# Optimization experiments

Hardware: AMD Instinct MI355X
Metric: run time of the kernel (lower is better)

Reference implementation:

```python
import math
import jax, jax.numpy as jnp
import numpy as np

N, S, E, H = 8, 1024, 768, 12  # batch, seq_len, n_embed, n_head


def setup_inputs() -> dict:
    key = jax.random.key(0)
    ks = jax.random.split(key, 10)
    s = 1.0 / math.sqrt(E)
    x = jax.random.normal(ks[0], (N, S, E), dtype=jnp.float32)
    # per-head full-width projections, stacked over heads: [H, E, E] (Linear weight layout [out, in])
    Wq = jax.random.normal(ks[1], (H, E, E), dtype=jnp.float32) * s
    Wk = jax.random.normal(ks[2], (H, E, E), dtype=jnp.float32) * s
    Wv = jax.random.normal(ks[3], (H, E, E), dtype=jnp.float32) * s
    bq = jax.random.normal(ks[4], (H, E), dtype=jnp.float32) * s
    bk = jax.random.normal(ks[5], (H, E), dtype=jnp.float32) * s
    bv = jax.random.normal(ks[6], (H, E), dtype=jnp.float32) * s
    Wc = jax.random.normal(ks[7], (E, H * E), dtype=jnp.float32) * (1.0 / math.sqrt(H * E))
    bc = jax.random.normal(ks[8], (E,), dtype=jnp.float32) * s
    return {"x": x, "Wq": Wq, "bq": bq, "Wk": Wk, "bk": bk, "Wv": Wv, "bv": bv, "Wc": Wc, "bc": bc}


def reference(x, Wq, bq, Wk, bk, Wv, bv, Wc, bc):
    # Full-width QKV per head: [H, N, S, E]
    q = jnp.einsum('nse,hde->hnsd', x, Wq) + bq[:, None, None, :]
    k = jnp.einsum('nse,hde->hnsd', x, Wk) + bk[:, None, None, :]
    v = jnp.einsum('nse,hde->hnsd', x, Wv) + bv[:, None, None, :]
    # scores scaled by sqrt(n_embed) (source quirk: full n_embed, not head_dim)
    scores = jnp.einsum('hnsd,hntd->hnst', q, k) / math.sqrt(E)
    causal = jnp.tril(jnp.ones((S, S), dtype=bool))
    scores = jnp.where(causal[None, None, :, :], scores, -jnp.inf)
    # dropout applied before softmax in source; p=0 (eval) -> identity
    attn = jax.nn.softmax(scores, axis=-1)
    heads = jnp.einsum('hnst,hntd->hnsd', attn, v)  # [H, N, S, E]
    concat = jnp.transpose(heads, (1, 2, 0, 3)).reshape(N, S, H * E)
    return concat @ Wc.T + bc
```

## Files before the change

kernel.cpp:

```cpp
#include <hip/hip_runtime.h>
#include <hip/hip_bf16.h>
#include <stdint.h>

#define SEQ    1024
#define NBAT   8
#define EMB    768
#define NHEAD  12
#define MROWS  (NBAT*SEQ)
#define SCALE_S 0.03608439182435161f

typedef unsigned short u16;
typedef __attribute__((ext_vector_type(8))) short bf16x8;
typedef __attribute__((ext_vector_type(4))) float f32x4;

typedef void __attribute__((address_space(1)))* gas_ptr;
typedef void __attribute__((address_space(3)))* las_ptr;

__device__ __forceinline__ void gload16(const void* g, void* l) {
  __builtin_amdgcn_global_load_lds((gas_ptr)(void*)g, (las_ptr)l, 16, 0, 0);
}

#define VMCNT0 asm volatile("s_waitcnt vmcnt(0)" ::: "memory")
#define VMCNT2 asm volatile("s_waitcnt vmcnt(2)" ::: "memory")
#define VMCNT4 asm volatile("s_waitcnt vmcnt(4)" ::: "memory")
#define LGKM0  asm volatile("s_waitcnt lgkmcnt(0)" ::: "memory")
#define BARRIER asm volatile("s_barrier" ::: "memory")

__device__ __forceinline__ u16 f2bf(float f) {
  union { float f; uint32_t u; } a; a.f = f;
  uint32_t r = a.u + 0x7fffu + ((a.u >> 16) & 1u);
  return (u16)(r >> 16);
}
__device__ __forceinline__ float bf2f(u16 b) {
  union { uint32_t u; float f; } c; c.u = (uint32_t)b << 16; return c.f;
}
__device__ __forceinline__ uint32_t pack2(float a, float b) {
  return (uint32_t)f2bf(a) | ((uint32_t)f2bf(b) << 16);
}

__global__ void k_cvt(const float* __restrict__ s, u16* __restrict__ d, long n) {
  long i = ((long)blockIdx.x*blockDim.x + threadIdx.x)*8;
  if (i >= n) return;
  float4 a = *(const float4*)(s+i);
  float4 b = *(const float4*)(s+i+4);
  uint4 o; o.x = pack2(a.x,a.y); o.y = pack2(a.z,a.w);
  o.z = pack2(b.x,b.y); o.w = pack2(b.z,b.w);
  *(uint4*)(d+i) = o;
}

__global__ void k_cvtT(const float* __restrict__ wq, const float* __restrict__ wk,
                       u16* __restrict__ dq, u16* __restrict__ dk, int Gi) {
  __shared__ float t[64][65];
  int z = blockIdx.z;
  const float* src = (z < Gi) ? wq + (size_t)z*EMB*EMB : wk + (size_t)(z-Gi)*EMB*EMB;
  u16* dst = (z < Gi) ? dq + (size_t)z*EMB*EMB : dk + (size_t)(z-Gi)*EMB*EMB;
  int d0 = blockIdx.x*64, e0 = blockIdx.y*64;
  int tt = threadIdx.x;
  int el = tt & 63, db = tt >> 6;
  #pragma unroll
  for (int p = 0; p < 16; ++p) {
    int dl = p*4 + db;
    t[dl][el] = src[(size_t)(d0+dl)*EMB + e0 + el];
  }
  __syncthreads();
  int dl2 = tt & 63, eb = tt >> 6;
  #pragma unroll
  for (int p = 0; p < 16; ++p) {
    int e2 = p*4 + eb;
    dst[(size_t)(e0+e2)*EMB + d0 + dl2] = f2bf(t[dl2][e2]);
  }
}

__global__ void k_cvtwc(const float* __restrict__ wc, u16* __restrict__ d, int Gi, int h0) {
  long ncol = (long)Gi*EMB;
  long i = ((long)blockIdx.x*blockDim.x + threadIdx.x)*4;
  if (i >= 768*ncol) return;
  long eo = i / ncol, c = i - eo*ncol;
  long g = c / EMB, dd = c - g*EMB;
  const float* s = wc + eo*(long)(NHEAD*EMB) + (h0+g)*EMB + dd;
  float4 a = *(const float4*)s;
  uint2 o; o.x = pack2(a.x,a.y); o.y = pack2(a.z,a.w);
  *(uint2*)(d+i) = o;
}

__global__ void k_mka(const u16* __restrict__ wkT, const float* __restrict__ bq,
                      float* __restrict__ a) {
  int g = blockIdx.y;
  int e = blockIdx.x*256 + threadIdx.x;
  const u16* row = wkT + (size_t)g*EMB*EMB + (size_t)e*EMB;
  const float* b = bq + (size_t)g*EMB;
  float s = 0.f;
  for (int d = 0; d < EMB; ++d) s += bf2f(row[d]) * b[d];
  a[(size_t)g*EMB + e] = s;
}

__global__ void k_mkv(const u16* __restrict__ xb, const float* __restrict__ a,
                      float* __restrict__ v) {
  int g = blockIdx.y;
  int w = threadIdx.x >> 6, l = threadIdx.x & 63;
  int i = blockIdx.x*8 + w;
  const u16* xr = xb + (size_t)i*EMB;
  const float* ag = a + (size_t)g*EMB;
  float s = 0.f;
  #pragma unroll
  for (int c = 0; c < 12; ++c) {
    int e = c*64 + l;
    s += bf2f(xr[e]) * ag[e];
  }
  s += __shfl_xor(s, 1); s += __shfl_xor(s, 2); s += __shfl_xor(s, 4);
  s += __shfl_xor(s, 8); s += __shfl_xor(s, 16); s += __shfl_xor(s, 32);
  if (l == 0) v[(size_t)g*MROWS + i] = s;
}

__global__ __launch_bounds__(512, 2) void k_gemm256(
    const u16* __restrict__ A, int lda,
    const u16* __restrict__ B, int ldb, int K,
    u16* __restrict__ Cb, long c_hs, int ldc,
    const float* __restrict__ bias, const float* __restrict__ bias2,
    int gsplit, int mode)
{
  __shared__ u16 lsA[2*16384];
  __shared__ u16 lsB[2*16384];

  int m0 = blockIdx.x * 256;
  int n0 = blockIdx.y * 256;
  int tid = threadIdx.x;
  int w = tid >> 6, l = tid & 63;
  int wr = w >> 2, wc = w & 3;

  const u16* gA = A + (size_t)(m0 + 32*w + (l>>3))*lda + (((l&7) ^ (l>>3)) << 3);
  const u16* gB = B + (size_t)(n0 + 32*w + (l>>3))*ldb + (((l&7) ^ (l>>3)) << 3);

#define STAGE256(t, buf) do { \
    int k0_ = (t)*64; \
    _Pragma("unroll") \
    for (int c_ = 0; c_ < 4; ++c_) \
      gload16(gA + (size_t)(c_*8)*lda + k0_, lsA + (buf)*16384 + (32*w + 8*c_)*64); \
    _Pragma("unroll") \
    for (int c_ = 0; c_ < 4; ++c_) \
      gload16(gB + (size_t)(c_*8)*ldb + k0_, lsB + (buf)*16384 + (32*w + 8*c_)*64); \
  } while(0)

  f32x4 acc[8][4];
  #pragma unroll
  for (int i = 0; i < 8; ++i)
    #pragma unroll
    for (int j = 0; j < 4; ++j) acc[i][j] = (f32x4)0.0f;

  int nt = K >> 6;
  STAGE256(0, 0);
  for (int t = 0; t < nt; ++t) {
    VMCNT0; BARRIER;
    if (t + 1 < nt) STAGE256(t+1, (t+1)&1);
    const u16* la = lsA + (t&1)*16384;
    const u16* lb = lsB + (t&1)*16384;
    #pragma unroll
    for (int ks = 0; ks < 2; ++ks) {
      int off = (((4*ks + (l>>4)) ^ (l&7)) << 3);
      bf16x8 af[8], bf_[4];
      #pragma unroll
      for (int fi = 0; fi < 8; ++fi)
        af[fi] = *(const bf16x8*)(la + (wr*128 + fi*16 + (l&15))*64 + off);
      #pragma unroll
      for (int fj = 0; fj < 4; ++fj)
        bf_[fj] = *(const bf16x8*)(lb + (wc*64 + fj*16 + (l&15))*64 + off);
      __builtin_amdgcn_s_setprio(1);
      #pragma unroll
      for (int fi = 0; fi < 8; ++fi)
        #pragma unroll
        for (int fj = 0; fj < 4; ++fj)
          acc[fi][fj] = __builtin_amdgcn_mfma_f32_16x16x32_bf16(af[fi], bf_[fj], acc[fi][fj], 0, 0, 0);
      __builtin_amdgcn_s_setprio(0);
    }
  }
#undef STAGE256

  if (mode == 0) {
    int s = n0 / 768;
    int dbase = n0 - s*768 + wc*64;
    const float* bsl = bias ? ((s < gsplit) ? bias + (size_t)s*768
                                            : bias2 + (size_t)(s - gsplit)*768)
                            : (const float*)0;
    u16* Cs = Cb + (size_t)s*c_hs;
    #pragma unroll
    for (int fj = 0; fj < 4; ++fj) {
      int dcol = dbase + fj*16 + (l&15);
      float bb = bsl ? bsl[dcol] : 0.f;
      #pragma unroll
      for (int fi = 0; fi < 8; ++fi) {
        #pragma unroll
        for (int r = 0; r < 4; ++r) {
          int row = m0 + wr*128 + fi*16 + (l>>4)*4 + r;
          Cs[(size_t)row*768 + dcol] = f2bf(acc[fi][fj][r] + bb);
        }
      }
    }
  } else {
    #pragma unroll
    for (int fi = 0; fi < 8; ++fi) {
      #pragma unroll
      for (int r = 0; r < 4; ++r) {
        int row = m0 + wr*128 + fi*16 + (l>>4)*4 + r;
        float bb = bias[row];
        #pragma unroll
        for (int fj = 0; fj < 4; ++fj) {
          int cbn = n0 + wc*64 + fj*16 + (l&15);
          Cb[(size_t)row*ldc + cbn] = f2bf(acc[fi][fj][r] + bb);
        }
      }
    }
  }
}

__global__ __launch_bounds__(256) void k_gemm(
    const u16* __restrict__ A, long a_hs, int lda,
    const u16* __restrict__ B, long b_hs, int ldb, int K,
    u16* Cb, float* Cf, long c_hs, int ldc,
    const float* __restrict__ bias, const float* __restrict__ bias2,
    long bias_hs, int gsplit, int mode, int swapxy)
{
  __shared__ u16 lsA[3*4096];
  __shared__ u16 lsB[3*4096];
  int g = blockIdx.z;
  const u16* Ag = A + (long)g*a_hs;
  const u16* Bg = B + (long)g*b_hs;
  int tm = swapxy ? blockIdx.y : blockIdx.x;
  int tn = swapxy ? blockIdx.x : blockIdx.y;
  int m0 = tm*128, n0 = tn*128;
  int tid = threadIdx.x;
  int w = tid >> 6, l = tid & 63;

  int srow = l >> 2;
  int scol = ((l & 3) ^ ((l >> 3) & 3)) * 8;
  const u16* ga0 = Ag + (long)(m0 + (2*w)*16   + srow)*lda + scol;
  const u16* ga1 = Ag + (long)(m0 + (2*w+1)*16 + srow)*lda + scol;
  const u16* gb0 = Bg + (long)(n0 + (2*w)*16   + srow)*ldb + scol;
  const u16* gb1 = Bg + (long)(n0 + (2*w+1)*16 + srow)*ldb + scol;

#define GSTAGE(k0, buf) do { \
    gload16(ga0 + (k0), lsA + (buf)*4096 + (2*w)*512); \
    gload16(ga1 + (k0), lsA + (buf)*4096 + (2*w+1)*512); \
    gload16(gb0 + (k0), lsB + (buf)*4096 + (2*w)*512); \
    gload16(gb1 + (k0), lsB + (buf)*4096 + (2*w+1)*512); \
  } while(0)

  f32x4 acc[4][4];
  #pragma unroll
  for (int i = 0; i < 4; ++i)
    #pragma unroll
    for (int j = 0; j < 4; ++j) acc[i][j] = (f32x4)0.0f;

  int wr = w >> 1, wc_ = w & 1;
  int frow = l & 15;
  int sp = (l >> 4) ^ ((frow >> 1) & 3);
  int aoff[4], boff[4];
  #pragma unroll
  for (int i = 0; i < 4; ++i) {
    aoff[i] = (wr*64 + i*16 + frow)*32 + sp*8;
    boff[i] = (wc_*64 + i*16 + frow)*32 + sp*8;
  }

  int nt = K >> 5;
  GSTAGE(0, 0);
  GSTAGE(32, 1);
  VMCNT4; BARRIER;
  int cur = 0;
  for (int t = 0; t < nt; ++t) {
    if (t + 2 < nt) {
      int nb = cur + 2; if (nb >= 3) nb -= 3;
      GSTAGE((t+2) << 5, nb);
    }
    const u16* la = lsA + cur*4096;
    const u16* lb = lsB + cur*4096;
    bf16x8 af[4], bfr[4];
    #pragma unroll
    for (int i = 0; i < 4; ++i) af[i] = *(const bf16x8*)(la + aoff[i]);
    #pragma unroll
    for (int j = 0; j < 4; ++j) bfr[j] = *(const bf16x8*)(lb + boff[j]);
    #pragma unroll
    for (int i = 0; i < 4; ++i)
      #pragma unroll
      for (int j = 0; j < 4; ++j)
        acc[i][j] = __builtin_amdgcn_mfma_f32_16x16x32_bf16(af[i], bfr[j], acc[i][j], 0, 0, 0);
    if (t + 2 < nt) { VMCNT4; } else { VMCNT0; }
    LGKM0; BARRIER;
    cur = (cur == 2) ? 0 : cur + 1;
  }
#undef GSTAGE

  u16* Cbg = Cb ? Cb + (long)g*c_hs : (u16*)0;
  const float* bsel = (g < gsplit) ? bias : bias2;
  long gi = (g < gsplit) ? g : g - gsplit;
  const float* bs = bsel ? bsel + gi*bias_hs : (const float*)0;
  int rl = (l >> 4)*4, cl = l & 15;
  #pragma unroll
  for (int i = 0; i < 4; ++i) {
    #pragma unroll
    for (int j = 0; j < 4; ++j) {
      int rb = m0 + wr*64 + i*16 + rl;
      int cb = n0 + wc_*64 + j*16 + cl;
      float cbv = 0.f;
      if ((mode == 0 || mode == 2) && bs) cbv = bs[cb];
      #pragma unroll
      for (int r = 0; r < 4; ++r) {
        int rr = rb + r;
        float v = acc[i][j][r];
        v += (mode == 1) ? bs[rr] : cbv;
        size_t idx = (size_t)rr*(size_t)ldc + cb;
        if (mode <= 1) Cbg[idx] = f2bf(v);
        else if (mode == 2) Cf[idx] = v;
        else Cf[idx] += v;
      }
    }
  }
}

__global__ __launch_bounds__(512, 2) void k_attn(
    const u16* __restrict__ qb, const u16* __restrict__ xkb,
    const u16* __restrict__ vtb, const float* __restrict__ vh,
    u16* __restrict__ hb, int ldh)
{
  __shared__ u16 kls[3*8192];
  __shared__ u16 vls[3*8192];
  __shared__ float s_t[64*68];
  __shared__ u16 p_t[64*64];
  __shared__ float e_s[64];

  int b = blockIdx.x;
  int xcd = b & 7, kk_ = b >> 3;
  int gn = xcd + 8*(kk_ >> 3), pair = kk_ & 7;
  int g = gn >> 3, n = gn & 7;

  const u16* Q  = qb  + (size_t)g*MROWS*EMB + (size_t)n*SEQ*EMB;
  const u16* Kp = xkb + (size_t)n*SEQ*EMB;
  const u16* Vt = vtb + (size_t)g*EMB*MROWS + (size_t)n*SEQ;
  const float* Vh = vh + (size_t)g*MROWS + (size_t)n*SEQ;
  u16* H = hb + (size_t)(n*SEQ)*ldh + (size_t)g*EMB;

  int tid = threadIdx.x;
  int w = tid >> 6, l = tid & 63;
  int qg = w >> 1;
  int cg = w & 1;
  int frow = l & 15;
  int fsw = frow & 7;
  int srow = tid >> 3;
  int sphys = tid & 7;
  int scol = ((sphys ^ (srow & 7)) << 3);

#define KSTAGE(base, pc, buf) do { \
    gload16((base) + (pc)*128,      kls + (buf)*8192 + w*512); \
    gload16((base) + (pc)*128 + 64, kls + (buf)*8192 + 4096 + w*512); \
  } while(0)
#define VSTAGE(vc, buf) do { \
    gload16(Vs + (size_t)((vc)*128)*MROWS,      vls + (buf)*8192 + w*512); \
    gload16(Vs + (size_t)((vc)*128 + 64)*MROWS, vls + (buf)*8192 + 4096 + w*512); \
  } while(0)

  for (int half = 0; half < 2; ++half) {
    int qt = half ? 15 - pair : pair;
    int q0 = qt * 64;
    int nt = qt + 1;

    f32x4 acc[6][4];
    #pragma unroll
    for (int i = 0; i < 6; ++i)
      #pragma unroll
      for (int j = 0; j < 4; ++j) acc[i][j] = (f32x4)0.0f;
    float m_reg = -1e30f, l_reg = 0.f;

    const u16* Qs = Q + (size_t)(q0 + srow)*EMB + scol;
    bf16x8 qreg[12][2];
    KSTAGE(Qs, 0, 0);
    KSTAGE(Qs, 1, 1);
    VMCNT2; BARRIER;
    #pragma unroll
    for (int pc = 0; pc < 6; ++pc) {
      if (pc < 4) KSTAGE(Qs, pc+2, (pc+2)%3);
      const u16* qb_ = kls + (pc%3)*8192;
      #pragma unroll
      for (int kk2 = 0; kk2 < 2; ++kk2)
        #pragma unroll
        for (int kkl = 0; kkl < 2; ++kkl)
          qreg[2*pc + kk2][kkl] = *(const bf16x8*)(qb_ + kk2*4096 + (qg*16 + frow)*64
                                                   + (((kkl*4 + (l>>4)) ^ fsw) << 3));
      if (pc < 4) { VMCNT2; } else if (pc == 4) { VMCNT0; }
      LGKM0; BARRIER;
    }

    for (int tt = 0; tt < nt; ++tt) {
      int t0 = tt*64;
      const u16* Ks = Kp + (size_t)(t0 + srow)*EMB + scol;
      const u16* Vs = Vt + (size_t)srow*MROWS + t0 + scol;
      float vv0 = Vh[t0 + cg*32 + frow];
      float vv1 = Vh[t0 + cg*32 + 16 + frow];
      if (tt == 0) { KSTAGE(Ks, 0, 0); KSTAGE(Ks, 1, 1); }
      VMCNT2; BARRIER;

      f32x4 sacc[2]; sacc[0] = (f32x4)0.0f; sacc[1] = (f32x4)0.0f;
      #pragma unroll
      for (int c = 0; c < 6; ++c) {
        if (c < 4)       KSTAGE(Ks, c+2, (c+2)%3);
        else if (c == 4) VSTAGE(0, 0);
        else             VSTAGE(1, 1);
        const u16* kb_ = kls + (c%3)*8192;
        __builtin_amdgcn_s_setprio(1);
        #pragma unroll
        for (int kk2 = 0; kk2 < 2; ++kk2) {
          #pragma unroll
          for (int kkl = 0; kkl < 2; ++kkl) {
            int so = ((kkl*4 + (l>>4)) ^ fsw) << 3;
            bf16x8 aq = qreg[2*c + kk2][kkl];
            #pragma unroll
            for (int cc = 0; cc < 2; ++cc) {
              bf16x8 bk_ = *(const bf16x8*)(kb_ + kk2*4096 + ((cg*2 + cc)*16 + frow)*64 + so);
              sacc[cc] = __builtin_amdgcn_mfma_f32_16x16x32_bf16(aq, bk_, sacc[cc], 0, 0, 0);
            }
          }
        }
        __builtin_amdgcn_s_setprio(0);
        if (c < 5) { VMCNT2; LGKM0; BARRIER; }
      }

      #pragma unroll
      for (int r = 0; r < 4; ++r) {
        s_t[(qg*16 + (l>>4)*4 + r)*68 + cg*32 + frow]      = (sacc[0][r] + vv0)*SCALE_S;
        s_t[(qg*16 + (l>>4)*4 + r)*68 + cg*32 + 16 + frow] = (sacc[1][r] + vv1)*SCALE_S;
      }
      LGKM0; BARRIER;
      {
        int qglob = q0 + srow;
        int cbase = t0 + sphys*8;
        float v[8]; float mx = -1e30f;
        #pragma unroll
        for (int j = 0; j < 8; ++j) {
          float s = s_t[srow*68 + sphys*8 + j];
          if (cbase + j > qglob) s = -1e30f;
          v[j] = s; mx = fmaxf(mx, s);
        }
        mx = fmaxf(mx, __shfl_xor(mx, 1));
        mx = fmaxf(mx, __shfl_xor(mx, 2));
        mx = fmaxf(mx, __shfl_xor(mx, 4));
        float mn = fmaxf(m_reg, mx);
        float esc = __expf(m_reg - mn);
        float ps = 0.f; u16 pk[8];
        #pragma unroll
        for (int j = 0; j < 8; ++j) { float p = __expf(v[j] - mn); ps += p; pk[j] = f2bf(p); }
        ps += __shfl_xor(ps, 1); ps += __shfl_xor(ps, 2); ps += __shfl_xor(ps, 4);
        l_reg = l_reg*esc + ps; m_reg = mn;
        if (sphys == 0) e_s[srow] = esc;
        uint4 pv;
        pv.x = (uint32_t)pk[0] | ((uint32_t)pk[1] << 16);
        pv.y = (uint32_t)pk[2] | ((uint32_t)pk[3] << 16);
        pv.z = (uint32_t)pk[4] | ((uint32_t)pk[5] << 16);
        pv.w = (uint32_t)pk[6] | ((uint32_t)pk[7] << 16);
        *(uint4*)(p_t + srow*64 + ((sphys ^ (srow & 7)) << 3)) = pv;
      }
      VMCNT2; LGKM0; BARRIER;
      float er[4];
      #pragma unroll
      for (int r = 0; r < 4; ++r) er[r] = e_s[qg*16 + (l>>4)*4 + r];
      #pragma unroll
      for (int i = 0; i < 6; ++i)
        #pragma unroll
        for (int j = 0; j < 4; ++j)
          #pragma unroll
          for (int r = 0; r < 4; ++r) acc[i][j][r] *= er[r];
      bf16x8 pa[2];
      #pragma unroll
      for (int kk = 0; kk < 2; ++kk)
        pa[kk] = *(const bf16x8*)(p_t + (qg*16 + frow)*64 + (((kk*4 + (l>>4)) ^ fsw) << 3));
      bool stage_next = (tt + 1 < nt);
      const u16* Ks2 = Kp + (size_t)(t0 + 64 + srow)*EMB + scol;
      #pragma unroll
      for (int c = 0; c < 6; ++c) {
        if (c < 4)            VSTAGE(c+2, (c+2)%3);
        else if (stage_next)  { if (c == 4) KSTAGE(Ks2, 0, 0); else KSTAGE(Ks2, 1, 1); }
        const u16* vb_ = vls + (c%3)*8192;
        __builtin_amdgcn_s_setprio(1);
        #pragma unroll
        for (int cf = 0; cf < 4; ++cf) {
          #pragma unroll
          for (int kk = 0; kk < 2; ++kk) {
            bf16x8 vbf = *(const bf16x8*)(vb_ + (cg*64 + cf*16 + frow)*64 + (((kk*4 + (l>>4)) ^ fsw) << 3));
            acc[c][cf] = __builtin_amdgcn_mfma_f32_16x16x32_bf16(pa[kk], vbf, acc[c][cf], 0, 0, 0);
          }
        }
        __builtin_amdgcn_s_setprio(0);
        if (c < 4)      { VMCNT2; LGKM0; BARRIER; }
        else if (c == 4){ if (stage_next) { VMCNT2; } else { VMCNT0; } LGKM0; BARRIER; }
      }
    }
    if (sphys == 0) e_s[srow] = l_reg;
    LGKM0; BARRIER;
    float linv[4];
    #pragma unroll
    for (int r = 0; r < 4; ++r) linv[r] = 1.0f / e_s[qg*16 + (l>>4)*4 + r];
    #pragma unroll
    for (int i = 0; i < 6; ++i)
      #pragma unroll
      for (int j = 0; j < 4; ++j) {
        int col = i*128 + cg*64 + j*16 + (l & 15);
        #pragma unroll
        for (int r = 0; r < 4; ++r) {
          int row = q0 + qg*16 + (l>>4)*4 + r;
          H[(size_t)row*ldh + col] = f2bf(acc[i][j][r]*linv[r]);
        }
      }
    BARRIER;
  }
#undef KSTAGE
#undef VSTAGE
}

extern "C" void kernel_launch(void* const* d_in, const int* in_sizes, int n_in,
                              void* d_out, int out_size, void* d_ws, size_t ws_size,
                              hipStream_t stream) {
  const float* x  = (const float*)d_in[0];
  const float* Wq = (const float*)d_in[1];
  const float* bq = (const float*)d_in[2];
  const float* Wk = (const float*)d_in[3];
  const float* bv = (const float*)d_in[6];
  const float* Wv = (const float*)d_in[5];
  const float* Wc = (const float*)d_in[7];
  const float* bc = (const float*)d_in[8];
  float* out = (float*)d_out;

  const size_t XB  = (size_t)MROWS*EMB*sizeof(u16);
  const size_t WHB = (size_t)EMB*EMB*sizeof(u16);
  const size_t VHB = (size_t)MROWS*sizeof(float);
  const size_t AB  = (size_t)EMB*sizeof(float);
  const size_t per_g = 3*WHB + 3*XB + VHB + AB;
  int G = 4;
  { int cands[4] = {4, 3, 2, 1};
    for (int ci = 0; ci < 4; ++ci) {
      G = cands[ci];
      if (XB + (size_t)G*per_g + 4096 <= ws_size) break;
    } }

  char* ws = (char*)d_ws;
  u16* xb  = (u16*)ws;  ws += XB;
  u16* wvb = (u16*)ws;  ws += (size_t)G*WHB;
  u16* wcb = (u16*)ws;  ws += (size_t)G*WHB;
  u16* mtb = (u16*)ws;  ws += (size_t)G*WHB;
  u16* yb  = (u16*)ws;  ws += (size_t)G*XB;
  u16* vtb = (u16*)ws;  ws += (size_t)G*XB;
  u16* hbf = (u16*)ws;  ws += (size_t)G*XB;
  float* vh = (float*)ws; ws += (size_t)G*VHB;
  float* ab = (float*)ws; ws += (size_t)G*AB;
  u16* wqT = hbf;
  u16* wkT = hbf + (size_t)G*EMB*EMB;

  k_cvt<<<dim3(3072), dim3(256), 0, stream>>>(x, xb, (long)MROWS*EMB);

  for (int h0 = 0; h0 < NHEAD; h0 += G) {
    int Gi = (G < NHEAD - h0) ? G : (NHEAD - h0);
    k_cvtT<<<dim3(12, 12, 2*Gi), dim3(256), 0, stream>>>(
        Wq + (size_t)h0*EMB*EMB, Wk + (size_t)h0*EMB*EMB, wqT, wkT, Gi);
    k_cvt<<<dim3((unsigned)((long)Gi*EMB*EMB/8/256)), dim3(256), 0, stream>>>(
        Wv + (size_t)h0*EMB*EMB, wvb, (long)Gi*EMB*EMB);
    k_cvtwc<<<dim3((unsigned)((768L*Gi*EMB/4)/256)), dim3(256), 0, stream>>>(Wc, wcb, Gi, h0);
    k_gemm<<<dim3(6, 6, Gi), dim3(256), 0, stream>>>(
        wkT, (long)EMB*EMB, EMB, wqT, (long)EMB*EMB, EMB, EMB,
        mtb, (float*)0, (long)EMB*EMB, EMB,
        (const float*)0, (const float*)0, 0L, 9999, 0, 0);
    k_mka<<<dim3(3, Gi), dim3(256), 0, stream>>>(wkT, bq + (size_t)h0*EMB, ab);
    k_mkv<<<dim3(1024, Gi), dim3(512), 0, stream>>>(xb, ab, vh);
    k_gemm256<<<dim3(32, 3*Gi), dim3(512), 0, stream>>>(
        xb, EMB, mtb, EMB, EMB,
        yb, (long)MROWS*EMB, 768,
        (const float*)0, (const float*)0, Gi, 0);
    k_gemm256<<<dim3(3*Gi, 32), dim3(512), 0, stream>>>(
        wvb, EMB, xb, EMB, EMB,
        vtb, 0L, MROWS,
        bv + (size_t)h0*EMB, (const float*)0, 9999, 1);
    k_attn<<<dim3(8*NBAT*Gi), dim3(512), 0, stream>>>(
        yb, xb, vtb, vh, hbf, Gi*EMB);
    k_gemm<<<dim3(64, 6, 1), dim3(256), 0, stream>>>(
        hbf, 0L, Gi*EMB, wcb, 0L, Gi*EMB, Gi*EMB,
        (u16*)0, out, 0L, EMB,
        (h0 == 0 ? bc : (const float*)0), (const float*)0, 0L, 9999,
        (h0 == 0 ? 2 : 3), 0);
  }
}
```

Measured before the change: 1.206 ms.

## Unify attention LDS into a 4-buffer pool with 256-wide chunks; hoist weight prep

The attention kernel moves from separate 3-stage K and V LDS rings of 128-wide chunks to one 4-buffer pool of 256-wide chunks. K and V stages rotate through it, and the next tile's K loads are issued during the softmax and PV phases, so there are fewer barriers per tile and more loads in flight. Separately, the weight conversions, the Wk^T·Wq product and the bias-vector preparation now run once for all 12 heads before the head-group loop instead of once per group. This takes more workspace, and the larger LDS footprint may reduce occupancy.

Measured after the change: 1.121 ms. 1.08x faster.

```diff
diff --git a/kernel.cpp b/kernel.cpp
--- a/kernel.cpp
+++ b/kernel.cpp
@@ -21,8 +21,8 @@
 }
 
 #define VMCNT0 asm volatile("s_waitcnt vmcnt(0)" ::: "memory")
-#define VMCNT2 asm volatile("s_waitcnt vmcnt(2)" ::: "memory")
 #define VMCNT4 asm volatile("s_waitcnt vmcnt(4)" ::: "memory")
+#define VMCNT8 asm volatile("s_waitcnt vmcnt(8)" ::: "memory")
 #define LGKM0  asm volatile("s_waitcnt lgkmcnt(0)" ::: "memory")
 #define BARRIER asm volatile("s_barrier" ::: "memory")
 
@@ -320,8 +320,7 @@
     const u16* __restrict__ vtb, const float* __restrict__ vh,
     u16* __restrict__ hb, int ldh)
 {
-  __shared__ u16 kls[3*8192];
-  __shared__ u16 vls[3*8192];
+  __shared__ u16 pool[4*16384];
   __shared__ float s_t[64*68];
   __shared__ u16 p_t[64*64];
   __shared__ float e_s[64];
@@ -339,27 +338,75 @@
 
   int tid = threadIdx.x;
   int w = tid >> 6, l = tid & 63;
-  int qg = w >> 1;
-  int cg = w & 1;
-  int frow = l & 15;
-  int fsw = frow & 7;
-  int srow = tid >> 3;
-  int sphys = tid & 7;
+  int qg = w >> 1, cg = w & 1;
+  int frow = l & 15, fsw = frow & 7;
+  int srow = tid >> 3, sphys = tid & 7;
   int scol = ((sphys ^ (srow & 7)) << 3);
 
-#define KSTAGE(base, pc, buf) do { \
-    gload16((base) + (pc)*128,      kls + (buf)*8192 + w*512); \
-    gload16((base) + (pc)*128 + 64, kls + (buf)*8192 + 4096 + w*512); \
-  } while(0)
-#define VSTAGE(vc, buf) do { \
-    gload16(Vs + (size_t)((vc)*128)*MROWS,      vls + (buf)*8192 + w*512); \
-    gload16(Vs + (size_t)((vc)*128 + 64)*MROWS, vls + (buf)*8192 + 4096 + w*512); \
+#define STG_K(kbase, ch, buf) do { \
+    const u16* s_ = (kbase) + (size_t)srow*EMB + (ch)*256 + scol; \
+    u16* d_ = pool + (buf)*16384 + w*512; \
+    gload16(s_,       d_); \
+    gload16(s_ + 64,  d_ + 4096); \
+    gload16(s_ + 128, d_ + 8192); \
+    gload16(s_ + 192, d_ + 12288); \
+  } while(0)
+#define STG_Q(ch, buf) do { \
+    const u16* s_ = Q + (size_t)(q0 + srow)*EMB + (ch)*256 + scol; \
+    u16* d_ = pool + (buf)*16384 + w*512; \
+    gload16(s_,       d_); \
+    gload16(s_ + 64,  d_ + 4096); \
+    gload16(s_ + 128, d_ + 8192); \
+    gload16(s_ + 192, d_ + 12288); \
+  } while(0)
+#define STG_V(ch, buf, t0v) do { \
+    const u16* s_ = Vt + (size_t)((ch)*256 + srow)*MROWS + (t0v) + scol; \
+    u16* d_ = pool + (buf)*16384 + w*512; \
+    gload16(s_,                      d_); \
+    gload16(s_ + (size_t)64*MROWS,   d_ + 4096); \
+    gload16(s_ + (size_t)128*MROWS,  d_ + 8192); \
+    gload16(s_ + (size_t)192*MROWS,  d_ + 12288); \
+  } while(0)
+#define RD_Q(ch, buf) do { \
+    const u16* qp_ = pool + (buf)*16384; \
+    _Pragma("unroll") for (int c2 = 0; c2 < 2; ++c2) \
+    _Pragma("unroll") for (int k2 = 0; k2 < 2; ++k2) \
+    _Pragma("unroll") for (int kl = 0; kl < 2; ++kl) \
+      qreg[(ch)*8 + c2*4 + k2*2 + kl] = *(const bf16x8*)(qp_ + c2*8192 + k2*4096 \
+          + (qg*16 + frow)*64 + (((kl*4 + (l>>4)) ^ fsw) << 3)); \
+  } while(0)
+#define QK_PH(ch, buf) do { \
+    const u16* kb_ = pool + (buf)*16384; \
+    __builtin_amdgcn_s_setprio(1); \
+    _Pragma("unroll") for (int c2 = 0; c2 < 2; ++c2) \
+    _Pragma("unroll") for (int k2 = 0; k2 < 2; ++k2) \
+    _Pragma("unroll") for (int kl = 0; kl < 2; ++kl) { \
+      int so = ((kl*4 + (l>>4)) ^ fsw) << 3; \
+      bf16x8 aq = qreg[(ch)*8 + c2*4 + k2*2 + kl]; \
+      _Pragma("unroll") for (int cc = 0; cc < 2; ++cc) { \
+        bf16x8 bk_ = *(const bf16x8*)(kb_ + c2*8192 + k2*4096 + ((cg*2 + cc)*16 + frow)*64 + so); \
+        sacc[cc] = __builtin_amdgcn_mfma_f32_16x16x32_bf16(aq, bk_, sacc[cc], 0, 0, 0); \
+      } } \
+    __builtin_amdgcn_s_setprio(0); \
+  } while(0)
+#define PV_PH(ch, buf) do { \
+    const u16* vb_ = pool + (buf)*16384; \
+    __builtin_amdgcn_s_setprio(1); \
+    _Pragma("unroll") for (int c2 = 0; c2 < 2; ++c2) \
+    _Pragma("unroll") for (int cf = 0; cf < 4; ++cf) \
+    _Pragma("unroll") for (int kk = 0; kk < 2; ++kk) { \
+      bf16x8 vbf = *(const bf16x8*)(vb_ + c2*8192 + (cg*64 + cf*16 + frow)*64 \
+          + (((kk*4 + (l>>4)) ^ fsw) << 3)); \
+      acc[(ch)*2 + c2][cf] = __builtin_amdgcn_mfma_f32_16x16x32_bf16(pa[kk], vbf, acc[(ch)*2 + c2][cf], 0, 0, 0); \
+    } \
+    __builtin_amdgcn_s_setprio(0); \
   } while(0)
 
   for (int half = 0; half < 2; ++half) {
     int qt = half ? 15 - pair : pair;
     int q0 = qt * 64;
-    int nt = qt + 1;
+    int ntk = qt + 1;
+    int qglob = q0 + srow;
 
     f32x4 acc[6][4];
     #pragma unroll
@@ -368,67 +415,35 @@
       for (int j = 0; j < 4; ++j) acc[i][j] = (f32x4)0.0f;
     float m_reg = -1e30f, l_reg = 0.f;
 
-    const u16* Qs = Q + (size_t)(q0 + srow)*EMB + scol;
-    bf16x8 qreg[12][2];
-    KSTAGE(Qs, 0, 0);
-    KSTAGE(Qs, 1, 1);
-    VMCNT2; BARRIER;
-    #pragma unroll
-    for (int pc = 0; pc < 6; ++pc) {
-      if (pc < 4) KSTAGE(Qs, pc+2, (pc+2)%3);
-      const u16* qb_ = kls + (pc%3)*8192;
-      #pragma unroll
-      for (int kk2 = 0; kk2 < 2; ++kk2)
-        #pragma unroll
-        for (int kkl = 0; kkl < 2; ++kkl)
-          qreg[2*pc + kk2][kkl] = *(const bf16x8*)(qb_ + kk2*4096 + (qg*16 + frow)*64
-                                                   + (((kkl*4 + (l>>4)) ^ fsw) << 3));
-      if (pc < 4) { VMCNT2; } else if (pc == 4) { VMCNT0; }
-      LGKM0; BARRIER;
-    }
-
-    for (int tt = 0; tt < nt; ++tt) {
+    bf16x8 qreg[24];
+    STG_Q(0, 0); STG_Q(1, 1); STG_Q(2, 2);
+    VMCNT8; BARRIER;
+    RD_Q(0, 0); STG_K(Kp, 0, 3); VMCNT8; LGKM0; BARRIER;
+    RD_Q(1, 1); STG_K(Kp, 1, 0); VMCNT8; LGKM0; BARRIER;
+    RD_Q(2, 2); STG_K(Kp, 2, 1); VMCNT8; LGKM0; BARRIER;
+
+    for (int tt = 0; tt < ntk; ++tt) {
       int t0 = tt*64;
-      const u16* Ks = Kp + (size_t)(t0 + srow)*EMB + scol;
-      const u16* Vs = Vt + (size_t)srow*MROWS + t0 + scol;
+      int p = tt & 1;
+      int bK0 = p?1:3, bK1 = p?2:0, bK2 = p?3:1;
+      int bV0 = p?0:2, bV1 = p?1:3, bV2 = p?2:0;
+      bool sn = (tt + 1 < ntk);
+      const u16* Kn = Kp + (size_t)(t0 + 64)*EMB;
       float vv0 = Vh[t0 + cg*32 + frow];
       float vv1 = Vh[t0 + cg*32 + 16 + frow];
-      if (tt == 0) { KSTAGE(Ks, 0, 0); KSTAGE(Ks, 1, 1); }
-      VMCNT2; BARRIER;
 
       f32x4 sacc[2]; sacc[0] = (f32x4)0.0f; sacc[1] = (f32x4)0.0f;
-      #pragma unroll
-      for (int c = 0; c < 6; ++c) {
-        if (c < 4)       KSTAGE(Ks, c+2, (c+2)%3);
-        else if (c == 4) VSTAGE(0, 0);
-        else             VSTAGE(1, 1);
-        const u16* kb_ = kls + (c%3)*8192;
-        __builtin_amdgcn_s_setprio(1);
-        #pragma unroll
-        for (int kk2 = 0; kk2 < 2; ++kk2) {
-          #pragma unroll
-          for (int kkl = 0; kkl < 2; ++kkl) {
-            int so = ((kkl*4 + (l>>4)) ^ fsw) << 3;
-            bf16x8 aq = qreg[2*c + kk2][kkl];
-            #pragma unroll
-            for (int cc = 0; cc < 2; ++cc) {
-              bf16x8 bk_ = *(const bf16x8*)(kb_ + kk2*4096 + ((cg*2 + cc)*16 + frow)*64 + so);
-              sacc[cc] = __builtin_amdgcn_mfma_f32_16x16x32_bf16(aq, bk_, sacc[cc], 0, 0, 0);
-            }
-          }
-        }
-        __builtin_amdgcn_s_setprio(0);
-        if (c < 5) { VMCNT2; LGKM0; BARRIER; }
-      }
-
+      STG_V(0, bV0, t0);  QK_PH(0, bK0);  VMCNT8; LGKM0; BARRIER;
+      STG_V(1, bV1, t0);  QK_PH(1, bK1);  VMCNT8; LGKM0; BARRIER;
+      STG_V(2, bV2, t0);  QK_PH(2, bK2);
       #pragma unroll
       for (int r = 0; r < 4; ++r) {
         s_t[(qg*16 + (l>>4)*4 + r)*68 + cg*32 + frow]      = (sacc[0][r] + vv0)*SCALE_S;
         s_t[(qg*16 + (l>>4)*4 + r)*68 + cg*32 + 16 + frow] = (sacc[1][r] + vv1)*SCALE_S;
       }
-      LGKM0; BARRIER;
+      VMCNT8; LGKM0; BARRIER;
+      if (sn) STG_K(Kn, 0, bK2);
       {
-        int qglob = q0 + srow;
         int cbase = t0 + sphys*8;
         float v[8]; float mx = -1e30f;
         #pragma unroll
@@ -444,7 +459,7 @@
         float esc = __expf(m_reg - mn);
         float ps = 0.f; u16 pk[8];
         #pragma unroll
-        for (int j = 0; j < 8; ++j) { float p = __expf(v[j] - mn); ps += p; pk[j] = f2bf(p); }
+        for (int j = 0; j < 8; ++j) { float ppv = __expf(v[j] - mn); ps += ppv; pk[j] = f2bf(ppv); }
         ps += __shfl_xor(ps, 1); ps += __shfl_xor(ps, 2); ps += __shfl_xor(ps, 4);
         l_reg = l_reg*esc + ps; m_reg = mn;
         if (sphys == 0) e_s[srow] = esc;
@@ -455,7 +470,8 @@
         pv.w = (uint32_t)pk[6] | ((uint32_t)pk[7] << 16);
         *(uint4*)(p_t + srow*64 + ((sphys ^ (srow & 7)) << 3)) = pv;
       }
-      VMCNT2; LGKM0; BARRIER;
+      if (sn) { VMCNT8; } else { VMCNT4; }
+      LGKM0; BARRIER;
       float er[4];
       #pragma unroll
       for (int r = 0; r < 4; ++r) er[r] = e_s[qg*16 + (l>>4)*4 + r];
@@ -469,27 +485,17 @@
       #pragma unroll
       for (int kk = 0; kk < 2; ++kk)
         pa[kk] = *(const bf16x8*)(p_t + (qg*16 + frow)*64 + (((kk*4 + (l>>4)) ^ fsw) << 3));
-      bool stage_next = (tt + 1 < nt);
-      const u16* Ks2 = Kp + (size_t)(t0 + 64 + srow)*EMB + scol;
-      #pragma unroll
-      for (int c = 0; c < 6; ++c) {
-        if (c < 4)            VSTAGE(c+2, (c+2)%3);
-        else if (stage_next)  { if (c == 4) KSTAGE(Ks2, 0, 0); else KSTAGE(Ks2, 1, 1); }
-        const u16* vb_ = vls + (c%3)*8192;
-        __builtin_amdgcn_s_setprio(1);
-        #pragma unroll
-        for (int cf = 0; cf < 4; ++cf) {
-          #pragma unroll
-          for (int kk = 0; kk < 2; ++kk) {
-            bf16x8 vbf = *(const bf16x8*)(vb_ + (cg*64 + cf*16 + frow)*64 + (((kk*4 + (l>>4)) ^ fsw) << 3));
-            acc[c][cf] = __builtin_amdgcn_mfma_f32_16x16x32_bf16(pa[kk], vbf, acc[c][cf], 0, 0, 0);
-          }
-        }
-        __builtin_amdgcn_s_setprio(0);
-        if (c < 4)      { VMCNT2; LGKM0; BARRIER; }
-        else if (c == 4){ if (stage_next) { VMCNT2; } else { VMCNT0; } LGKM0; BARRIER; }
-      }
+      PV_PH(0, bV0);  VMCNT8; LGKM0; BARRIER;
+      if (sn) STG_K(Kn, 1, bV0);
+      PV_PH(1, bV1);
+      if (sn) { VMCNT8; } else { VMCNT0; }
+      LGKM0; BARRIER;
+      if (sn) STG_K(Kn, 2, bV1);
+      PV_PH(2, bV2);
+      if (sn) { VMCNT8; } else { VMCNT0; }
+      LGKM0; BARRIER;
     }
+
     if (sphys == 0) e_s[srow] = l_reg;
     LGKM0; BARRIER;
     float linv[4];
@@ -508,8 +514,12 @@
       }
     BARRIER;
   }
-#undef KSTAGE
-#undef VSTAGE
+#undef STG_K
+#undef STG_Q
+#undef STG_V
+#undef RD_Q
+#undef QK_PH
+#undef PV_PH
 }
 
 extern "C" void kernel_launch(void* const* d_in, const int* in_sizes, int n_in,
@@ -529,54 +539,49 @@
   const size_t WHB = (size_t)EMB*EMB*sizeof(u16);
   const size_t VHB = (size_t)MROWS*sizeof(float);
   const size_t AB  = (size_t)EMB*sizeof(float);
-  const size_t per_g = 3*WHB + 3*XB + VHB + AB;
+  const size_t fixed = XB + 36*WHB + 12*(VHB + AB) + 8192;
   int G = 4;
-  { int cands[4] = {4, 3, 2, 1};
-    for (int ci = 0; ci < 4; ++ci) {
-      G = cands[ci];
-      if (XB + (size_t)G*per_g + 4096 <= ws_size) break;
-    } }
+  while (G > 2 && fixed + (size_t)G*3*XB > ws_size) --G;
 
   char* ws = (char*)d_ws;
   u16* xb  = (u16*)ws;  ws += XB;
-  u16* wvb = (u16*)ws;  ws += (size_t)G*WHB;
-  u16* wcb = (u16*)ws;  ws += (size_t)G*WHB;
-  u16* mtb = (u16*)ws;  ws += (size_t)G*WHB;
+  u16* wvb = (u16*)ws;  ws += 12*WHB;
+  u16* wcb = (u16*)ws;  ws += 12*WHB;
+  u16* mtb = (u16*)ws;  ws += 12*WHB;
+  float* vh = (float*)ws; ws += 12*VHB;
+  float* ab = (float*)ws; ws += 12*AB;
   u16* yb  = (u16*)ws;  ws += (size_t)G*XB;
   u16* vtb = (u16*)ws;  ws += (size_t)G*XB;
   u16* hbf = (u16*)ws;  ws += (size_t)G*XB;
-  float* vh = (float*)ws; ws += (size_t)G*VHB;
-  float* ab = (float*)ws; ws += (size_t)G*AB;
   u16* wqT = hbf;
-  u16* wkT = hbf + (size_t)G*EMB*EMB;
+  u16* wkT = vtb;
 
   k_cvt<<<dim3(3072), dim3(256), 0, stream>>>(x, xb, (long)MROWS*EMB);
+  k_cvtT<<<dim3(12, 12, 24), dim3(256), 0, stream>>>(Wq, Wk, wqT, wkT, 12);
+  k_cvt<<<dim3((unsigned)((12L*EMB*EMB/8)/256)), dim3(256), 0, stream>>>(
+      Wv, wvb, 12L*EMB*EMB);
+  k_cvtwc<<<dim3((unsigned)((768L*12*EMB/4)/256)), dim3(256), 0, stream>>>(Wc, wcb, 12, 0);
+  k_gemm<<<dim3(6, 6, 12), dim3(256), 0, stream>>>(
+      wkT, (long)EMB*EMB, EMB, wqT, (long)EMB*EMB, EMB, EMB,
+      mtb, (float*)0, (long)EMB*EMB, EMB,
+      (const float*)0, (const float*)0, 0L, 9999, 0, 0);
+  k_mka<<<dim3(3, 12), dim3(256), 0, stream>>>(wkT, bq, ab);
+  k_mkv<<<dim3(1024, 12), dim3(512), 0, stream>>>(xb, ab, vh);
 
   for (int h0 = 0; h0 < NHEAD; h0 += G) {
     int Gi = (G < NHEAD - h0) ? G : (NHEAD - h0);
-    k_cvtT<<<dim3(12, 12, 2*Gi), dim3(256), 0, stream>>>(
-        Wq + (size_t)h0*EMB*EMB, Wk + (size_t)h0*EMB*EMB, wqT, wkT, Gi);
-    k_cvt<<<dim3((unsigned)((long)Gi*EMB*EMB/8/256)), dim3(256), 0, stream>>>(
-        Wv + (size_t)h0*EMB*EMB, wvb, (long)Gi*EMB*EMB);
-    k_cvtwc<<<dim3((unsigned)((768L*Gi*EMB/4)/256)), dim3(256), 0, stream>>>(Wc, wcb, Gi, h0);
-    k_gemm<<<dim3(6, 6, Gi), dim3(256), 0, stream>>>(
-        wkT, (long)EMB*EMB, EMB, wqT, (long)EMB*EMB, EMB, EMB,
-        mtb, (float*)0, (long)EMB*EMB, EMB,
-        (const float*)0, (const float*)0, 0L, 9999, 0, 0);
-    k_mka<<<dim3(3, Gi), dim3(256), 0, stream>>>(wkT, bq + (size_t)h0*EMB, ab);
-    k_mkv<<<dim3(1024, Gi), dim3(512), 0, stream>>>(xb, ab, vh);
     k_gemm256<<<dim3(32, 3*Gi), dim3(512), 0, stream>>>(
-        xb, EMB, mtb, EMB, EMB,
+        xb, EMB, mtb + (size_t)h0*EMB*EMB, EMB, EMB,
         yb, (long)MROWS*EMB, 768,
         (const float*)0, (const float*)0, Gi, 0);
     k_gemm256<<<dim3(3*Gi, 32), dim3(512), 0, stream>>>(
-        wvb, EMB, xb, EMB, EMB,
+        wvb + (size_t)h0*EMB*EMB, EMB, xb, EMB, EMB,
         vtb, 0L, MROWS,
         bv + (size_t)h0*EMB, (const float*)0, 9999, 1);
     k_attn<<<dim3(8*NBAT*Gi), dim3(512), 0, stream>>>(
-        yb, xb, vtb, vh, hbf, Gi*EMB);
+        yb, xb, vtb, vh + (size_t)h0*MROWS, hbf, Gi*EMB);
     k_gemm<<<dim3(64, 6, 1), dim3(256), 0, stream>>>(
-        hbf, 0L, Gi*EMB, wcb, 0L, Gi*EMB, Gi*EMB,
+        hbf, 0L, Gi*EMB, wcb + (size_t)h0*EMB, 0L, NHEAD*EMB, Gi*EMB,
         (u16*)0, out, 0L, EMB,
         (h0 == 0 ? bc : (const float*)0), (const float*)0, 0L, 9999,
         (h0 == 0 ? 2 : 3), 0);
```

## Hoist per-head weight prep out of group loop and merge Y/V GEMMs

Applied to the files above, without the earlier changes.

All weight conversions, the Wk^T·Wq product, and the bias-derived vectors now run once for all 12 heads before the group loop, so the loop no longer issues many small launches per group. The two large per-group GEMMs (Y projection and transposed V) are merged into one launch using blockIdx.z to pick an argument set, which doubles the grid and should fill the device better. In exchange the workspace must hold full 12-head weight buffers, which may shrink G, and the transposed weights now alias the vtb/hbf buffers.

After: 1.009 ms. 1.2x faster.

```diff
diff --git a/kernel.cpp b/kernel.cpp
--- a/kernel.cpp
+++ b/kernel.cpp
@@ -112,33 +112,37 @@
   if (l == 0) v[(size_t)g*MROWS + i] = s;
 }
 
-__global__ __launch_bounds__(512, 2) void k_gemm256(
-    const u16* __restrict__ A, int lda,
-    const u16* __restrict__ B, int ldb, int K,
-    u16* __restrict__ Cb, long c_hs, int ldc,
-    const float* __restrict__ bias, const float* __restrict__ bias2,
-    int gsplit, int mode)
+struct Gemm256Args {
+  const u16* A; int lda;
+  const u16* B; int ldb; int K;
+  u16* Cb; long c_hs; int ldc;
+  const float* bias; const float* bias2;
+  int gsplit; int mode; int swap;
+};
+
+__global__ __launch_bounds__(512, 2) void k_gemm256d(Gemm256Args p0, Gemm256Args p1)
 {
   __shared__ u16 lsA[2*16384];
   __shared__ u16 lsB[2*16384];
 
-  int m0 = blockIdx.x * 256;
-  int n0 = blockIdx.y * 256;
+  const Gemm256Args P = blockIdx.z ? p1 : p0;
+  int m0 = (P.swap ? blockIdx.y : blockIdx.x) * 256;
+  int n0 = (P.swap ? blockIdx.x : blockIdx.y) * 256;
   int tid = threadIdx.x;
   int w = tid >> 6, l = tid & 63;
   int wr = w >> 2, wc = w & 3;
 
-  const u16* gA = A + (size_t)(m0 + 32*w + (l>>3))*lda + (((l&7) ^ (l>>3)) << 3);
-  const u16* gB = B + (size_t)(n0 + 32*w + (l>>3))*ldb + (((l&7) ^ (l>>3)) << 3);
+  const u16* gA = P.A + (size_t)(m0 + 32*w + (l>>3))*P.lda + (((l&7) ^ (l>>3)) << 3);
+  const u16* gB = P.B + (size_t)(n0 + 32*w + (l>>3))*P.ldb + (((l&7) ^ (l>>3)) << 3);
 
 #define STAGE256(t, buf) do { \
     int k0_ = (t)*64; \
     _Pragma("unroll") \
     for (int c_ = 0; c_ < 4; ++c_) \
-      gload16(gA + (size_t)(c_*8)*lda + k0_, lsA + (buf)*16384 + (32*w + 8*c_)*64); \
+      gload16(gA + (size_t)(c_*8)*P.lda + k0_, lsA + (buf)*16384 + (32*w + 8*c_)*64); \
     _Pragma("unroll") \
     for (int c_ = 0; c_ < 4; ++c_) \
-      gload16(gB + (size_t)(c_*8)*ldb + k0_, lsB + (buf)*16384 + (32*w + 8*c_)*64); \
+      gload16(gB + (size_t)(c_*8)*P.ldb + k0_, lsB + (buf)*16384 + (32*w + 8*c_)*64); \
   } while(0)
 
   f32x4 acc[8][4];
@@ -147,7 +151,7 @@
     #pragma unroll
     for (int j = 0; j < 4; ++j) acc[i][j] = (f32x4)0.0f;
 
-  int nt = K >> 6;
+  int nt = P.K >> 6;
   STAGE256(0, 0);
   for (int t = 0; t < nt; ++t) {
     VMCNT0; BARRIER;
@@ -175,13 +179,13 @@
   }
 #undef STAGE256
 
-  if (mode == 0) {
+  if (P.mode == 0) {
     int s = n0 / 768;
     int dbase = n0 - s*768 + wc*64;
-    const float* bsl = bias ? ((s < gsplit) ? bias + (size_t)s*768
-                                            : bias2 + (size_t)(s - gsplit)*768)
-                            : (const float*)0;
-    u16* Cs = Cb + (size_t)s*c_hs;
+    const float* bsl = P.bias ? ((s < P.gsplit) ? P.bias + (size_t)s*768
+                                                : P.bias2 + (size_t)(s - P.gsplit)*768)
+                              : (const float*)0;
+    u16* Cs = P.Cb + (size_t)s*P.c_hs;
     #pragma unroll
     for (int fj = 0; fj < 4; ++fj) {
       int dcol = dbase + fj*16 + (l&15);
@@ -201,11 +205,11 @@
       #pragma unroll
       for (int r = 0; r < 4; ++r) {
         int row = m0 + wr*128 + fi*16 + (l>>4)*4 + r;
-        float bb = bias[row];
+        float bb = P.bias[row];
         #pragma unroll
         for (int fj = 0; fj < 4; ++fj) {
           int cbn = n0 + wc*64 + fj*16 + (l&15);
-          Cb[(size_t)row*ldc + cbn] = f2bf(acc[fi][fj][r] + bb);
+          P.Cb[(size_t)row*P.ldc + cbn] = f2bf(acc[fi][fj][r] + bb);
         }
       }
     }
@@ -529,54 +533,48 @@
   const size_t WHB = (size_t)EMB*EMB*sizeof(u16);
   const size_t VHB = (size_t)MROWS*sizeof(float);
   const size_t AB  = (size_t)EMB*sizeof(float);
-  const size_t per_g = 3*WHB + 3*XB + VHB + AB;
+  const size_t fixed = XB + 36*WHB + 12*(VHB + AB) + 8192;
   int G = 4;
-  { int cands[4] = {4, 3, 2, 1};
-    for (int ci = 0; ci < 4; ++ci) {
-      G = cands[ci];
-      if (XB + (size_t)G*per_g + 4096 <= ws_size) break;
-    } }
+  while (G > 2 && fixed + (size_t)G*3*XB > ws_size) --G;
 
   char* ws = (char*)d_ws;
   u16* xb  = (u16*)ws;  ws += XB;
-  u16* wvb = (u16*)ws;  ws += (size_t)G*WHB;
-  u16* wcb = (u16*)ws;  ws += (size_t)G*WHB;
-  u16* mtb = (u16*)ws;  ws += (size_t)G*WHB;
+  u16* wvb = (u16*)ws;  ws += 12*WHB;
+  u16* wcb = (u16*)ws;  ws += 12*WHB;
+  u16* mtb = (u16*)ws;  ws += 12*WHB;
+  float* vh = (float*)ws; ws += 12*VHB;
+  float* ab = (float*)ws; ws += 12*AB;
   u16* yb  = (u16*)ws;  ws += (size_t)G*XB;
   u16* vtb = (u16*)ws;  ws += (size_t)G*XB;
   u16* hbf = (u16*)ws;  ws += (size_t)G*XB;
-  float* vh = (float*)ws; ws += (size_t)G*VHB;
-  float* ab = (float*)ws; ws += (size_t)G*AB;
   u16* wqT = hbf;
-  u16* wkT = hbf + (size_t)G*EMB*EMB;
+  u16* wkT = vtb;
 
   k_cvt<<<dim3(3072), dim3(256), 0, stream>>>(x, xb, (long)MROWS*EMB);
+  k_cvtT<<<dim3(12, 12, 24), dim3(256), 0, stream>>>(Wq, Wk, wqT, wkT, 12);
+  k_cvt<<<dim3((unsigned)((12L*EMB*EMB/8)/256)), dim3(256), 0, stream>>>(
+      Wv, wvb, 12L*EMB*EMB);
+  k_cvtwc<<<dim3((unsigned)((768L*12*EMB/4)/256)), dim3(256), 0, stream>>>(Wc, wcb, 12, 0);
+  k_gemm<<<dim3(6, 6, 12), dim3(256), 0, stream>>>(
+      wkT, (long)EMB*EMB, EMB, wqT, (long)EMB*EMB, EMB, EMB,
+      mtb, (float*)0, (long)EMB*EMB, EMB,
+      (const float*)0, (const float*)0, 0L, 9999, 0, 0);
+  k_mka<<<dim3(3, 12), dim3(256), 0, stream>>>(wkT, bq, ab);
+  k_mkv<<<dim3(1024, 12), dim3(512), 0, stream>>>(xb, ab, vh);
 
   for (int h0 = 0; h0 < NHEAD; h0 += G) {
     int Gi = (G < NHEAD - h0) ? G : (NHEAD - h0);
-    k_cvtT<<<dim3(12, 12, 2*Gi), dim3(256), 0, stream>>>(
-        Wq + (size_t)h0*EMB*EMB, Wk + (size_t)h0*EMB*EMB, wqT, wkT, Gi);
-    k_cvt<<<dim3((unsigned)((long)Gi*EMB*EMB/8/256)), dim3(256), 0, stream>>>(
-        Wv + (size_t)h0*EMB*EMB, wvb, (long)Gi*EMB*EMB);
-    k_cvtwc<<<dim3((unsigned)((768L*Gi*EMB/4)/256)), dim3(256), 0, stream>>>(Wc, wcb, Gi, h0);
-    k_gemm<<<dim3(6, 6, Gi), dim3(256), 0, stream>>>(
-        wkT, (long)EMB*EMB, EMB, wqT, (long)EMB*EMB, EMB, EMB,
-        mtb, (float*)0, (long)EMB*EMB, EMB,
-        (const float*)0, (const float*)0, 0L, 9999, 0, 0);
-    k_mka<<<dim3(3, Gi), dim3(256), 0, stream>>>(wkT, bq + (size_t)h0*EMB, ab);
-    k_mkv<<<dim3(1024, Gi), dim3(512), 0, stream>>>(xb, ab, vh);
-    k_gemm256<<<dim3(32, 3*Gi), dim3(512), 0, stream>>>(
-        xb, EMB, mtb, EMB, EMB,
-        yb, (long)MROWS*EMB, 768,
-        (const float*)0, (const float*)0, Gi, 0);
-    k_gemm256<<<dim3(3*Gi, 32), dim3(512), 0, stream>>>(
-        wvb, EMB, xb, EMB, EMB,
-        vtb, 0L, MROWS,
-        bv + (size_t)h0*EMB, (const float*)0, 9999, 1);
+    Gemm256Args ay = { xb, EMB, mtb + (size_t)h0*EMB*EMB, EMB, EMB,
+                       yb, (long)MROWS*EMB, 768,
+                       (const float*)0, (const float*)0, Gi, 0, 0 };
+    Gemm256Args av = { wvb + (size_t)h0*EMB*EMB, EMB, xb, EMB, EMB,
+                       vtb, 0L, MROWS,
+                       bv + (size_t)h0*EMB, (const float*)0, 9999, 1, 1 };
+    k_gemm256d<<<dim3(32, 3*Gi, 2), dim3(512), 0, stream>>>(ay, av);
     k_attn<<<dim3(8*NBAT*Gi), dim3(512), 0, stream>>>(
-        yb, xb, vtb, vh, hbf, Gi*EMB);
+        yb, xb, vtb, vh + (size_t)h0*MROWS, hbf, Gi*EMB);
     k_gemm<<<dim3(64, 6, 1), dim3(256), 0, stream>>>(
-        hbf, 0L, Gi*EMB, wcb, 0L, Gi*EMB, Gi*EMB,
+        hbf, 0L, Gi*EMB, wcb + (size_t)h0*EMB, 0L, NHEAD*EMB, Gi*EMB,
         (u16*)0, out, 0L, EMB,
         (h0 == 0 ? bc : (const float*)0), (const float*)0, 0L, 9999,
         (h0 == 0 ? 2 : 3), 0);
```
